# Kernel tuning notes

Hardware: AMD Instinct MI355X
Metric: run time of the kernel (lower is better)

Reference implementation:

```python
import jax, jax.numpy as jnp
import numpy as np

N_USER, N_ITEM = 100000, 50000
E, L = 640000, 200000
F0, F1, F2 = 128, 128, 64


def _mean_agg(x_src, src, dst, n_dst):
    # gather messages from source nodes, mean-aggregate onto destination nodes
    msg = x_src[src]                                            # [E, F]
    s = jax.ops.segment_sum(msg, dst, num_segments=n_dst)       # [n_dst, F]
    cnt = jax.ops.segment_sum(jnp.ones((src.shape[0], 1), x_src.dtype), dst,
                              num_segments=n_dst)               # [n_dst, 1]
    return s / jnp.maximum(cnt, 1.0)


def _sage(x_src, x_dst, src, dst, n_dst, Wl, b, Wr):
    # PyG SAGEConv: lin_l(mean_aggr(x_src)) + lin_r(x_dst)
    agg = _mean_agg(x_src, src, dst, n_dst)
    return agg @ Wl + b + x_dst @ Wr


def setup_inputs() -> dict:
    key = jax.random.key(0)
    ks = jax.random.split(key, 20)
    inp = {}
    inp['x_user'] = jax.random.normal(ks[0], (N_USER, F0), jnp.float32)
    inp['x_item'] = jax.random.normal(ks[1], (N_ITEM, F0), jnp.float32)
    inp['src_u'] = jax.random.randint(ks[2], (E,), 0, N_USER)
    inp['dst_i'] = jax.random.randint(ks[3], (E,), 0, N_ITEM)
    inp['el_src'] = jax.random.randint(ks[4], (L,), 0, N_USER)
    inp['el_dst'] = jax.random.randint(ks[5], (L,), 0, N_ITEM)
    # SAGEConv params per edge type per layer: Wl (neighbor), bias, Wr (root)
    def w(k, fi, fo):
        return jax.random.normal(k, (fi, fo), jnp.float32) * (1.0 / np.sqrt(fi))
    inp['Wl_ui1'] = w(ks[6], F0, F1);  inp['b_ui1'] = jnp.zeros((F1,), jnp.float32)
    inp['Wr_ui1'] = w(ks[7], F0, F1)
    inp['Wl_iu1'] = w(ks[8], F0, F1);  inp['b_iu1'] = jnp.zeros((F1,), jnp.float32)
    inp['Wr_iu1'] = w(ks[9], F0, F1)
    inp['Wl_ui2'] = w(ks[10], F1, F2); inp['b_ui2'] = jnp.zeros((F2,), jnp.float32)
    inp['Wr_ui2'] = w(ks[11], F1, F2)
    inp['Wl_iu2'] = w(ks[12], F1, F2); inp['b_iu2'] = jnp.zeros((F2,), jnp.float32)
    inp['Wr_iu2'] = w(ks[13], F1, F2)
    return inp


def reference(x_user, x_item, src_u, dst_i, el_src, el_dst,
              Wl_ui1, b_ui1, Wr_ui1, Wl_iu1, b_iu1, Wr_iu1,
              Wl_ui2, b_ui2, Wr_ui2, Wl_iu2, b_iu2, Wr_iu2):
    # layer 1 (to_hetero: one SAGEConv per edge type; relu per node type; eval -> no dropout)
    h_i1 = jax.nn.relu(_sage(x_user, x_item, src_u, dst_i, N_ITEM, Wl_ui1, b_ui1, Wr_ui1))
    h_u1 = jax.nn.relu(_sage(x_item, x_user, dst_i, src_u, N_USER, Wl_iu1, b_iu1, Wr_iu1))
    # layer 2
    h_i2 = _sage(h_u1, h_i1, src_u, dst_i, N_ITEM, Wl_ui2, b_ui2, Wr_ui2)
    h_u2 = _sage(h_i1, h_u1, dst_i, src_u, N_USER, Wl_iu2, b_iu2, Wr_iu2)
    # LPsimple_classif: gather endpoints, elementwise product, sum over features
    pred = (h_u2[el_src] * h_i2[el_dst]).sum(axis=-1)           # [L]
    return pred
```

## Files before the change

### kernel.cpp

```cpp
#include <hip/hip_runtime.h>

#define NUSER 100000
#define NITEM 50000
#define NEDGE 640000
#define NLINK 200000
#define GI 49
#define GU 98

typedef unsigned int  uint;
typedef unsigned short ushort_t;
typedef __attribute__((ext_vector_type(8))) short bf16x8;
typedef __attribute__((ext_vector_type(4))) float f32x4;
typedef __attribute__((ext_vector_type(4))) uint  u32x4;

__device__ __forceinline__ ushort_t f2bf(float f) {
    uint u = __float_as_uint(f);
    u += 0x7FFFu + ((u >> 16) & 1u);
    return (ushort_t)(u >> 16);
}
__device__ __forceinline__ float bf2f(ushort_t h) { return __uint_as_float(((uint)h) << 16); }
__device__ __forceinline__ float lo16f(uint u) { return __uint_as_float(u << 16); }
__device__ __forceinline__ float hi16f(uint u) { return __uint_as_float(u & 0xFFFF0000u); }

__global__ __launch_bounds__(256) void countw_kernel(
    const int* __restrict__ src, const int* __restrict__ dst,
    int* __restrict__ cnt_u, int* __restrict__ cnt_i,
    const float* __restrict__ Wl0, const float* __restrict__ Wr0,
    const float* __restrict__ Wl1, const float* __restrict__ Wr1,
    const float* __restrict__ Wl2, const float* __restrict__ Wr2,
    const float* __restrict__ Wl3, const float* __restrict__ Wr3,
    ushort_t* __restrict__ Bh0, ushort_t* __restrict__ Bl0,
    ushort_t* __restrict__ Bh1, ushort_t* __restrict__ Bl1,
    ushort_t* __restrict__ Bh2, ushort_t* __restrict__ Bl2,
    ushort_t* __restrict__ Bh3, ushort_t* __restrict__ Bl3)
{
    if (blockIdx.x < 2500) {
        int e = blockIdx.x * 256 + threadIdx.x;
        if (e >= NEDGE) return;
        atomicAdd(&cnt_u[src[e]], 1);
        atomicAdd(&cnt_i[dst[e]], 1);
        return;
    }
    int b = blockIdx.x - 2500;
    const float *Wl, *Wr; ushort_t *Bh, *Bl; int FO, t;
    if (b < 16)      { Wl = Wl0; Wr = Wr0; Bh = Bh0; Bl = Bl0; FO = 128; t = b * 256 + threadIdx.x; }
    else if (b < 32) { Wl = Wl1; Wr = Wr1; Bh = Bh1; Bl = Bl1; FO = 128; t = (b - 16) * 256 + threadIdx.x; }
    else if (b < 40) { Wl = Wl2; Wr = Wr2; Bh = Bh2; Bl = Bl2; FO = 64;  t = (b - 32) * 256 + threadIdx.x; }
    else             { Wl = Wl3; Wr = Wr3; Bh = Bh3; Bl = Bl3; FO = 64;  t = (b - 40) * 256 + threadIdx.x; }
    int lane = t & 63, ks = (t >> 6) & 3, nt = t >> 8;
    int col = nt * 16 + (lane & 15);
    int k0 = ks * 32 + (lane >> 4) * 8;
    const float* W = (col < FO) ? Wl : Wr;
    int cc = (col < FO) ? col : col - FO;
#pragma unroll
    for (int j = 0; j < 8; ++j) {
        float v = W[(size_t)(k0 + j) * FO + cc];
        ushort_t h = f2bf(v);
        Bh[(size_t)t * 8 + j] = h;
        Bl[(size_t)t * 8 + j] = f2bf(v - bf2f(h));
    }
}

__global__ __launch_bounds__(256) void scan1_kernel(
    const int* __restrict__ cnt_i, const int* __restrict__ cnt_u,
    int* __restrict__ head_i, int* __restrict__ head_u,
    int* __restrict__ bsum_i, int* __restrict__ bsum_u)
{
    __shared__ int sh[256];
    int b = blockIdx.x, t = threadIdx.x;
    const int* cnt; int* head; int* bsum; int n, cb;
    if (b < GI) { cnt = cnt_i; head = head_i; bsum = bsum_i; n = NITEM; cb = b; }
    else        { cnt = cnt_u; head = head_u; bsum = bsum_u; n = NUSER; cb = b - GI; }
    int base = cb * 1024 + t * 4;
    int4 v = {0, 0, 0, 0};
    if (base + 3 < n) v = *(const int4*)(cnt + base);
    else {
        if (base + 0 < n) v.x = cnt[base + 0];
        if (base + 1 < n) v.y = cnt[base + 1];
        if (base + 2 < n) v.z = cnt[base + 2];
    }
    int s = v.x + v.y + v.z + v.w;
    sh[t] = s;
    __syncthreads();
    for (int o = 1; o < 256; o <<= 1) {
        int a = (t >= o) ? sh[t - o] : 0;
        __syncthreads();
        sh[t] += a;
        __syncthreads();
    }
    int excl = sh[t] - s;
    if (t == 255) bsum[cb] = sh[255];
    if (base + 0 < n) head[base + 0] = excl;
    if (base + 1 < n) head[base + 1] = excl + v.x;
    if (base + 2 < n) head[base + 2] = excl + v.x + v.y;
    if (base + 3 < n) head[base + 3] = excl + v.x + v.y + v.z;
}

__global__ __launch_bounds__(256) void scan23_kernel(
    int* __restrict__ head_i, int* __restrict__ head_u,
    const int* __restrict__ bsum_i, const int* __restrict__ bsum_u)
{
    __shared__ int sh[256];
    int b = blockIdx.x, t = threadIdx.x;
    int* head; const int* bsum; int n, cb;
    if (b < GI) { head = head_i; bsum = bsum_i; n = NITEM; cb = b; }
    else        { head = head_u; bsum = bsum_u; n = NUSER; cb = b - GI; }
    sh[t] = (t < cb) ? bsum[t] : 0;
    __syncthreads();
    for (int o = 128; o >= 1; o >>= 1) {
        if (t < o) sh[t] += sh[t + o];
        __syncthreads();
    }
    int add = sh[0];
    int base = cb * 1024 + t * 4;
#pragma unroll
    for (int k = 0; k < 4; ++k)
        if (base + k < n) head[base + k] += add;
}

#define FCHUNK 2048
#define FNCH   313
#define NBG1   4688
__global__ __launch_bounds__(256) void gemmfill_kernel(
    const float* __restrict__ xu, const float* __restrict__ xi,
    const ushort_t* __restrict__ Bh0, const ushort_t* __restrict__ Bl0,
    const ushort_t* __restrict__ Bh1, const ushort_t* __restrict__ Bl1,
    ushort_t* __restrict__ y0, ushort_t* __restrict__ z0,
    ushort_t* __restrict__ y1, ushort_t* __restrict__ z1,
    const int* __restrict__ src, const int* __restrict__ dst,
    int* __restrict__ head_i, int* __restrict__ head_u,
    int* __restrict__ nbr_i, int* __restrict__ nbr_u)
{
    if (blockIdx.x >= NBG1) {
        int b = blockIdx.x - NBG1;
        int pass = b / (2 * FNCH);
        int rem  = b % (2 * FNCH);
        int dir  = rem / FNCH;
        int base = (rem % FNCH) * FCHUNK;
        int e_end = min(base + FCHUNK, NEDGE);
        if (dir == 0) {
            int lo = pass * (NITEM / 8), hi = lo + NITEM / 8;
            for (int e = base + threadIdx.x; e < e_end; e += 256) {
                int d = dst[e];
                if (d >= lo && d < hi) nbr_i[atomicAdd(&head_i[d], 1)] = src[e];
            }
        } else {
            int lo = pass * (NUSER / 8), hi = lo + NUSER / 8;
            for (int e = base + threadIdx.x; e < e_end; e += 256) {
                int s = src[e];
                if (s >= lo && s < hi) nbr_u[atomicAdd(&head_u[s], 1)] = dst[e];
            }
        }
        return;
    }

    __shared__ u32x4 ashH[32][16];
    __shared__ u32x4 ashL[32][16];
    const int tid = threadIdx.x;
    const float* A; const ushort_t *Bh, *Bl; ushort_t *ymsg, *zout; int n, row0;
    if ((int)blockIdx.x < 3125) { A = xu; Bh = Bh0; Bl = Bl0; ymsg = y0; zout = z0; n = NUSER; row0 = blockIdx.x * 32; }
    else { A = xi; Bh = Bh1; Bl = Bl1; ymsg = y1; zout = z1; n = NITEM; row0 = (blockIdx.x - 3125) * 32; }

#pragma unroll
    for (int i = 0; i < 2; ++i) {
        int idx = i * 256 + tid;
        int row = idx >> 4, ch = idx & 15;
        int grow = row0 + row;
        f32x4 f0 = {0.f, 0.f, 0.f, 0.f}, f1 = {0.f, 0.f, 0.f, 0.f};
        if (grow < n) {
            const f32x4* p = (const f32x4*)(A + (size_t)grow * 128 + ch * 8);
            f0 = p[0]; f1 = p[1];
        }
        float e[8];
#pragma unroll
        for (int j = 0; j < 4; ++j) { e[j] = f0[j]; e[4 + j] = f1[j]; }
        uint hv[4], lv[4];
#pragma unroll
        for (int j = 0; j < 4; ++j) {
            ushort_t h0 = f2bf(e[2 * j]), h1 = f2bf(e[2 * j + 1]);
            hv[j] = (uint)h0 | ((uint)h1 << 16);
            ushort_t l0 = f2bf(e[2 * j] - bf2f(h0)), l1 = f2bf(e[2 * j + 1] - bf2f(h1));
            lv[j] = (uint)l0 | ((uint)l1 << 16);
        }
        int sc = ch ^ (row & 7);
        u32x4 hq = {hv[0], hv[1], hv[2], hv[3]};
        u32x4 lq = {lv[0], lv[1], lv[2], lv[3]};
        ashH[row][sc] = hq;
        ashL[row][sc] = lq;
    }
    __syncthreads();

    const int lane = tid & 63, wv = tid >> 6;
    const int lr = lane & 15, lg = lane >> 4;
    const int colbase = wv * 64;
    f32x4 acc[2][4];
#pragma unroll
    for (int rt = 0; rt < 2; ++rt)
#pragma unroll
        for (int ct = 0; ct < 4; ++ct) { f32x4 zz = {0.f, 0.f, 0.f, 0.f}; acc[rt][ct] = zz; }

#pragma unroll
    for (int ks = 0; ks < 4; ++ks) {
        bf16x8 ah[2], al[2];
#pragma unroll
        for (int rt = 0; rt < 2; ++rt) {
            int row = rt * 16 + lr;
            int pos = (ks * 4 + lg) ^ (row & 7);
            ah[rt] = __builtin_bit_cast(bf16x8, ashH[row][pos]);
            al[rt] = __builtin_bit_cast(bf16x8, ashL[row][pos]);
        }
#pragma unroll
        for (int ct = 0; ct < 4; ++ct) {
            int nt = (colbase >> 4) + ct;
            size_t off = ((size_t)(nt * 4 + ks) * 64 + lane) * 8;
            bf16x8 bh = __builtin_bit_cast(bf16x8, *(const u32x4*)(Bh + off));
            bf16x8 bl = __builtin_bit_cast(bf16x8, *(const u32x4*)(Bl + off));
#pragma unroll
            for (int rt = 0; rt < 2; ++rt) {
                acc[rt][ct] = __builtin_amdgcn_mfma_f32_16x16x32_bf16(ah[rt], bh, acc[rt][ct], 0, 0, 0);
                acc[rt][ct] = __builtin_amdgcn_mfma_f32_16x16x32_bf16(ah[rt], bl, acc[rt][ct], 0, 0, 0);
                acc[rt][ct] = __builtin_amdgcn_mfma_f32_16x16x32_bf16(al[rt], bh, acc[rt][ct], 0, 0, 0);
            }
        }
    }

#pragma unroll
    for (int rt = 0; rt < 2; ++rt)
#pragma unroll
        for (int ct = 0; ct < 4; ++ct) {
            int col = colbase + ct * 16 + lr;
            bool ism = col < 128;
            ushort_t* dstp = ism ? ymsg : zout;
            int cc = ism ? col : col - 128;
#pragma unroll
            for (int r = 0; r < 4; ++r) {
                int row = row0 + rt * 16 + lg * 4 + r;
                if (row < n) dstp[(size_t)row * 128 + cc] = f2bf(acc[rt][ct][r]);
            }
        }
}

__global__ __launch_bounds__(256) void gemm2_kernel(
    const ushort_t* __restrict__ A0, const ushort_t* __restrict__ A1,
    const ushort_t* __restrict__ Bh0, const ushort_t* __restrict__ Bl0,
    const ushort_t* __restrict__ Bh1, const ushort_t* __restrict__ Bl1,
    ushort_t* __restrict__ y0, ushort_t* __restrict__ z0,
    ushort_t* __restrict__ y1, ushort_t* __restrict__ z1,
    int n0, int n1, int nb0)
{
    __shared__ u32x4 ashH[32][16];
    const int tid = threadIdx.x;
    const ushort_t* A; const ushort_t *Bh, *Bl; ushort_t *ymsg, *zout; int n, row0;
    if ((int)blockIdx.x < nb0) { A = A0; Bh = Bh0; Bl = Bl0; ymsg = y0; zout = z0; n = n0; row0 = blockIdx.x * 32; }
    else { A = A1; Bh = Bh1; Bl = Bl1; ymsg = y1; zout = z1; n = n1; row0 = (blockIdx.x - nb0) * 32; }

#pragma unroll
    for (int i = 0; i < 2; ++i) {
        int idx = i * 256 + tid;
        int row = idx >> 4, ch = idx & 15;
        int grow = row0 + row;
        u32x4 q = {0u, 0u, 0u, 0u};
        if (grow < n) q = *(const u32x4*)(A + (size_t)grow * 128 + ch * 8);
        ashH[row][ch ^ (row & 7)] = q;
    }
    __syncthreads();

    const int lane = tid & 63, wv = tid >> 6;
    const int lr = lane & 15, lg = lane >> 4;
    const int colbase = wv * 32;
    f32x4 acc[2][2];
#pragma unroll
    for (int rt = 0; rt < 2; ++rt)
#pragma unroll
        for (int ct = 0; ct < 2; ++ct) { f32x4 zz = {0.f, 0.f, 0.f, 0.f}; acc[rt][ct] = zz; }

#pragma unroll
    for (int ks = 0; ks < 4; ++ks) {
        bf16x8 ah[2];
#pragma unroll
        for (int rt = 0; rt < 2; ++rt) {
            int row = rt * 16 + lr;
            int pos = (ks * 4 + lg) ^ (row & 7);
            ah[rt] = __builtin_bit_cast(bf16x8, ashH[row][pos]);
        }
#pragma unroll
        for (int ct = 0; ct < 2; ++ct) {
            int nt = (colbase >> 4) + ct;
            size_t off = ((size_t)(nt * 4 + ks) * 64 + lane) * 8;
            bf16x8 bh = __builtin_bit_cast(bf16x8, *(const u32x4*)(Bh + off));
            bf16x8 bl = __builtin_bit_cast(bf16x8, *(const u32x4*)(Bl + off));
#pragma unroll
            for (int rt = 0; rt < 2; ++rt) {
                acc[rt][ct] = __builtin_amdgcn_mfma_f32_16x16x32_bf16(ah[rt], bh, acc[rt][ct], 0, 0, 0);
                acc[rt][ct] = __builtin_amdgcn_mfma_f32_16x16x32_bf16(ah[rt], bl, acc[rt][ct], 0, 0, 0);
            }
        }
    }

#pragma unroll
    for (int rt = 0; rt < 2; ++rt)
#pragma unroll
        for (int ct = 0; ct < 2; ++ct) {
            int col = colbase + ct * 16 + lr;
            bool ism = col < 64;
            ushort_t* dstp = ism ? ymsg : zout;
            int cc = ism ? col : col - 64;
#pragma unroll
            for (int r = 0; r < 4; ++r) {
                int row = row0 + rt * 16 + lg * 4 + r;
                if (row < n) dstp[(size_t)row * 64 + cc] = f2bf(acc[rt][ct][r]);
            }
        }
}

__global__ __launch_bounds__(256) void gather1_kernel(
    const ushort_t* __restrict__ ymsg_u, const ushort_t* __restrict__ ymsg_i,
    const int* __restrict__ nbr_i, const int* __restrict__ head_i, const int* __restrict__ cnt_i,
    const int* __restrict__ nbr_u, const int* __restrict__ head_u, const int* __restrict__ cnt_u,
    const ushort_t* __restrict__ z_i, const ushort_t* __restrict__ z_u,
    const float* __restrict__ b_ui, const float* __restrict__ b_iu,
    ushort_t* __restrict__ h1_i, ushort_t* __restrict__ h1_u)
{
    int w = (blockIdx.x << 2) + (threadIdx.x >> 6);
    const ushort_t *ym, *z; const int *nbr, *head, *cnt; const float* bias;
    ushort_t* hout; int node;
    if (w < NITEM) { ym = ymsg_u; nbr = nbr_i; head = head_i; cnt = cnt_i; z = z_i; bias = b_ui; hout = h1_i; node = w; }
    else if (w < NITEM + NUSER) { ym = ymsg_i; nbr = nbr_u; head = head_u; cnt = cnt_u; z = z_u; bias = b_iu; hout = h1_u; node = w - NITEM; }
    else return;
    int lane = threadIdx.x & 63;
    int c = cnt[node], end = head[node];
    int j = end - c;
    const uint* Y = (const uint*)ym;
    float ax = 0.f, ay = 0.f;
    for (; j + 7 < end; j += 8) {
        uint u0 = Y[(size_t)nbr[j + 0] * 64 + lane];
        uint u1 = Y[(size_t)nbr[j + 1] * 64 + lane];
        uint u2 = Y[(size_t)nbr[j + 2] * 64 + lane];
        uint u3 = Y[(size_t)nbr[j + 3] * 64 + lane];
        uint u4 = Y[(size_t)nbr[j + 4] * 64 + lane];
        uint u5 = Y[(size_t)nbr[j + 5] * 64 + lane];
        uint u6 = Y[(size_t)nbr[j + 6] * 64 + lane];
        uint u7 = Y[(size_t)nbr[j + 7] * 64 + lane];
        ax += lo16f(u0) + lo16f(u1) + lo16f(u2) + lo16f(u3)
            + lo16f(u4) + lo16f(u5) + lo16f(u6) + lo16f(u7);
        ay += hi16f(u0) + hi16f(u1) + hi16f(u2) + hi16f(u3)
            + hi16f(u4) + hi16f(u5) + hi16f(u6) + hi16f(u7);
    }
    for (; j + 1 < end; j += 2) {
        uint u0 = Y[(size_t)nbr[j + 0] * 64 + lane];
        uint u1 = Y[(size_t)nbr[j + 1] * 64 + lane];
        ax += lo16f(u0) + lo16f(u1);
        ay += hi16f(u0) + hi16f(u1);
    }
    if (j < end) {
        uint u0 = Y[(size_t)nbr[j] * 64 + lane];
        ax += lo16f(u0); ay += hi16f(u0);
    }
    float m = 1.f / fmaxf((float)c, 1.f);
    uint zu = ((const uint*)z)[(size_t)node * 64 + lane];
    float vx = fmaxf(ax * m + lo16f(zu) + bias[lane * 2], 0.f);
    float vy = fmaxf(ay * m + hi16f(zu) + bias[lane * 2 + 1], 0.f);
    ((uint*)hout)[(size_t)node * 64 + lane] = (uint)f2bf(vx) | ((uint)f2bf(vy) << 16);
}

__global__ __launch_bounds__(256) void gather2_kernel(
    const ushort_t* __restrict__ ymsg_u, const ushort_t* __restrict__ ymsg_i,
    const int* __restrict__ nbr_i, const int* __restrict__ head_i, const int* __restrict__ cnt_i,
    const int* __restrict__ nbr_u, const int* __restrict__ head_u, const int* __restrict__ cnt_u,
    const ushort_t* __restrict__ z_i, const ushort_t* __restrict__ z_u,
    const float* __restrict__ b_ui, const float* __restrict__ b_iu,
    ushort_t* __restrict__ h2_i, ushort_t* __restrict__ h2_u)
{
    int w = (blockIdx.x << 2) + (threadIdx.x >> 6);
    const ushort_t *ym, *z; const int *nbr, *head, *cnt; const float* bias;
    ushort_t* hout; int node;
    if (w < NITEM) { ym = ymsg_u; nbr = nbr_i; head = head_i; cnt = cnt_i; z = z_i; bias = b_ui; hout = h2_i; node = w; }
    else if (w < NITEM + NUSER) { ym = ymsg_i; nbr = nbr_u; head = head_u; cnt = cnt_u; z = z_u; bias = b_iu; hout = h2_u; node = w - NITEM; }
    else return;
    int lane = threadIdx.x & 63;
    int c = cnt[node], end = head[node];
    int j = end - c;
    float a = 0.f;
    for (; j + 7 < end; j += 8) {
        a += bf2f(ym[(size_t)nbr[j + 0] * 64 + lane]) + bf2f(ym[(size_t)nbr[j + 1] * 64 + lane])
           + bf2f(ym[(size_t)nbr[j + 2] * 64 + lane]) + bf2f(ym[(size_t)nbr[j + 3] * 64 + lane])
           + bf2f(ym[(size_t)nbr[j + 4] * 64 + lane]) + bf2f(ym[(size_t)nbr[j + 5] * 64 + lane])
           + bf2f(ym[(size_t)nbr[j + 6] * 64 + lane]) + bf2f(ym[(size_t)nbr[j + 7] * 64 + lane]);
    }
    for (; j + 1 < end; j += 2)
        a += bf2f(ym[(size_t)nbr[j] * 64 + lane]) + bf2f(ym[(size_t)nbr[j + 1] * 64 + lane]);
    if (j < end) a += bf2f(ym[(size_t)nbr[j] * 64 + lane]);
    float m = 1.f / fmaxf((float)c, 1.f);
    float v = a * m + bf2f(z[(size_t)node * 64 + lane]) + bias[lane];
    hout[(size_t)node * 64 + lane] = f2bf(v);
}

__global__ __launch_bounds__(256) void predict_kernel(
    const int* __restrict__ el_src, const int* __restrict__ el_dst,
    const ushort_t* __restrict__ hu, const ushort_t* __restrict__ hi,
    float* __restrict__ out)
{
    int l = (blockIdx.x << 2) + (threadIdx.x >> 6);
    if (l >= NLINK) return;
    int lane = threadIdx.x & 63;
    int u = el_src[l];
    int it = el_dst[l];
    float v = bf2f(hu[(size_t)u * 64 + lane]) * bf2f(hi[(size_t)it * 64 + lane]);
#pragma unroll
    for (int o = 32; o >= 1; o >>= 1) v += __shfl_down(v, o, 64);
    if (lane == 0) out[l] = v;
}

extern "C" void kernel_launch(void* const* d_in, const int* in_sizes, int n_in,
                              void* d_out, int out_size, void* d_ws, size_t ws_size,
                              hipStream_t stream) {
    const float* x_user = (const float*)d_in[0];
    const float* x_item = (const float*)d_in[1];
    const int*   src_u  = (const int*)d_in[2];
    const int*   dst_i  = (const int*)d_in[3];
    const int*   el_src = (const int*)d_in[4];
    const int*   el_dst = (const int*)d_in[5];
    const float* Wl_ui1 = (const float*)d_in[6];
    const float* b_ui1  = (const float*)d_in[7];
    const float* Wr_ui1 = (const float*)d_in[8];
    const float* Wl_iu1 = (const float*)d_in[9];
    const float* b_iu1  = (const float*)d_in[10];
    const float* Wr_iu1 = (const float*)d_in[11];
    const float* Wl_ui2 = (const float*)d_in[12];
    const float* b_ui2  = (const float*)d_in[13];
    const float* Wr_ui2 = (const float*)d_in[14];
    const float* Wl_iu2 = (const float*)d_in[15];
    const float* b_iu2  = (const float*)d_in[16];
    const float* Wr_iu2 = (const float*)d_in[17];
    float* out = (float*)d_out;

    int* iw     = (int*)d_ws;
    int* cnt_i  = iw;
    int* cnt_u  = iw + 50000;
    int* bsum_i = iw + 150000;
    int* bsum_u = iw + 150064;
    int* head_i = iw + 150192;
    int* head_u = iw + 200192;
    int* nbr_i  = iw + 300192;
    int* nbr_u  = iw + 940192;
    char* W8 = (char*)d_ws;
    size_t off = 6320768;
    ushort_t* Bh1u = (ushort_t*)(W8 + off); off += 65536;
    ushort_t* Bl1u = (ushort_t*)(W8 + off); off += 65536;
    ushort_t* Bh1i = (ushort_t*)(W8 + off); off += 65536;
    ushort_t* Bl1i = (ushort_t*)(W8 + off); off += 65536;
    ushort_t* Bh2u = (ushort_t*)(W8 + off); off += 32768;
    ushort_t* Bl2u = (ushort_t*)(W8 + off); off += 32768;
    ushort_t* Bh2i = (ushort_t*)(W8 + off); off += 32768;
    ushort_t* Bl2i = (ushort_t*)(W8 + off); off += 32768;
    ushort_t* h1_u = (ushort_t*)(W8 + off); off += (size_t)NUSER * 128 * 2;
    ushort_t* h1_i = (ushort_t*)(W8 + off); off += (size_t)NITEM * 128 * 2;
    size_t YB = off;
    ushort_t* ymsg_u = (ushort_t*)(W8 + YB);
    ushort_t* ymsg_i = (ushort_t*)(W8 + YB + 25600000);
    ushort_t* z_u    = (ushort_t*)(W8 + YB + 38400000);
    ushort_t* z_i    = (ushort_t*)(W8 + YB + 64000000);
    ushort_t* ymsg2_u = (ushort_t*)(W8 + YB);
    ushort_t* ymsg2_i = (ushort_t*)(W8 + YB + 12800000);
    ushort_t* z2_u    = (ushort_t*)(W8 + YB + 19200000);
    ushort_t* z2_i    = (ushort_t*)(W8 + YB + 32000000);
    ushort_t* h2_u    = (ushort_t*)(W8 + YB + 38400000);
    ushort_t* h2_i    = (ushort_t*)(W8 + YB + 51200000);

    hipMemsetAsync(d_ws, 0, 150000 * sizeof(int), stream);

    countw_kernel<<<2548, 256, 0, stream>>>(
        src_u, dst_i, cnt_u, cnt_i,
        Wl_ui1, Wr_iu1, Wl_iu1, Wr_ui1, Wl_ui2, Wr_iu2, Wl_iu2, Wr_ui2,
        Bh1u, Bl1u, Bh1i, Bl1i, Bh2u, Bl2u, Bh2i, Bl2i);

    scan1_kernel<<<GI + GU, 256, 0, stream>>>(cnt_i, cnt_u, head_i, head_u, bsum_i, bsum_u);
    scan23_kernel<<<GI + GU, 256, 0, stream>>>(head_i, head_u, bsum_i, bsum_u);

    gemmfill_kernel<<<NBG1 + 8 * 2 * FNCH, 256, 0, stream>>>(
        x_user, x_item, Bh1u, Bl1u, Bh1i, Bl1i,
        ymsg_u, z_u, ymsg_i, z_i,
        src_u, dst_i, head_i, head_u, nbr_i, nbr_u);

    gather1_kernel<<<(NITEM + NUSER) / 4, 256, 0, stream>>>(
        ymsg_u, ymsg_i, nbr_i, head_i, cnt_i, nbr_u, head_u, cnt_u,
        z_i, z_u, b_ui1, b_iu1, h1_i, h1_u);

    gemm2_kernel<<<3125 + 1563, 256, 0, stream>>>(
        h1_u, h1_i, Bh2u, Bl2u, Bh2i, Bl2i,
        ymsg2_u, z2_u, ymsg2_i, z2_i, NUSER, NITEM, 3125);
    gather2_kernel<<<(NITEM + NUSER) / 4, 256, 0, stream>>>(
        ymsg2_u, ymsg2_i, nbr_i, head_i, cnt_i, nbr_u, head_u, cnt_u,
        z2_i, z2_u, b_ui2, b_iu2, h2_i, h2_u);

    predict_kernel<<<NLINK / 4, 256, 0, stream>>>(el_src, el_dst, h2_u, h2_i, out);
}
```

Before: 353.5 us.

## Make GEMM blocks persistent over 128 rows with register-resident weights and prefetch

Both GEMM kernels now use 512-thread blocks, each looping over four 32-row sub-tiles (128 rows total). The split-bf16 weight fragments are loaded into registers once per block instead of being reloaded per 32-row tile, and the next sub-tile's activations are prefetched while the current one runs through MFMA. The edge-fill path uses larger chunks and 512-thread strides to match. Weight fragments held in registers raise VGPR pressure, which may lower occupancy, and the grid shrinks to about 1173 GEMM blocks.

```diff
diff --git a/kernel.cpp b/kernel.cpp
--- a/kernel.cpp
+++ b/kernel.cpp
@@ -6,6 +6,11 @@
 #define NLINK 200000
 #define GI 49
 #define GU 98
+#define NBU1 782
+#define NBI1 391
+#define NBG1 (NBU1 + NBI1)
+#define FCHUNK 4096
+#define FNCH 157
 
 typedef unsigned int  uint;
 typedef unsigned short ushort_t;
@@ -118,10 +123,127 @@
         if (base + k < n) head[base + k] += add;
 }
 
-#define FCHUNK 2048
-#define FNCH   313
-#define NBG1   4688
-__global__ __launch_bounds__(256) void gemmfill_kernel(
+template <int NO, bool ASPLIT>
+__device__ __forceinline__ void gemm_body(
+    const void* __restrict__ A_,
+    const ushort_t* __restrict__ Bh, const ushort_t* __restrict__ Bl,
+    ushort_t* __restrict__ ymsg, ushort_t* __restrict__ zout,
+    int n, int row0, u32x4 (*ashH)[16], u32x4 (*ashL)[16])
+{
+    constexpr int CT = NO / 128;
+    constexpr int FO = NO / 2;
+    const int tid = threadIdx.x;
+    const int lane = tid & 63, wv = tid >> 6;
+    const int lr = lane & 15, lg = lane >> 4;
+    const int row = tid >> 4, ch = tid & 15;
+
+    bf16x8 bfh[4][CT], bfl[4][CT];
+#pragma unroll
+    for (int ks = 0; ks < 4; ++ks)
+#pragma unroll
+        for (int ct = 0; ct < CT; ++ct) {
+            size_t boff = ((size_t)((wv * CT + ct) * 4 + ks) * 64 + lane) * 8;
+            bfh[ks][ct] = __builtin_bit_cast(bf16x8, *(const u32x4*)(Bh + boff));
+            bfl[ks][ct] = __builtin_bit_cast(bf16x8, *(const u32x4*)(Bl + boff));
+        }
+
+    f32x4 c0 = {0.f, 0.f, 0.f, 0.f}, c1 = {0.f, 0.f, 0.f, 0.f};
+    u32x4 cq = {0u, 0u, 0u, 0u};
+    {
+        int grow = row0 + row;
+        if (grow < n) {
+            if (ASPLIT) {
+                const f32x4* p = (const f32x4*)((const float*)A_ + (size_t)grow * 128 + ch * 8);
+                c0 = p[0]; c1 = p[1];
+            } else {
+                cq = *(const u32x4*)((const ushort_t*)A_ + (size_t)grow * 128 + ch * 8);
+            }
+        }
+    }
+
+#pragma unroll
+    for (int st = 0; st < 4; ++st) {
+        int sc = ch ^ (row & 7);
+        if (ASPLIT) {
+            float e[8];
+#pragma unroll
+            for (int j = 0; j < 4; ++j) { e[j] = c0[j]; e[4 + j] = c1[j]; }
+            uint hv[4], lv[4];
+#pragma unroll
+            for (int j = 0; j < 4; ++j) {
+                ushort_t h0 = f2bf(e[2 * j]), h1 = f2bf(e[2 * j + 1]);
+                hv[j] = (uint)h0 | ((uint)h1 << 16);
+                ushort_t l0 = f2bf(e[2 * j] - bf2f(h0)), l1 = f2bf(e[2 * j + 1] - bf2f(h1));
+                lv[j] = (uint)l0 | ((uint)l1 << 16);
+            }
+            u32x4 hq = {hv[0], hv[1], hv[2], hv[3]};
+            u32x4 lq = {lv[0], lv[1], lv[2], lv[3]};
+            ashH[row][sc] = hq;
+            ashL[row][sc] = lq;
+        } else {
+            ashH[row][sc] = cq;
+        }
+        __syncthreads();
+
+        if (st < 3) {
+            c0 = f32x4{0.f, 0.f, 0.f, 0.f}; c1 = f32x4{0.f, 0.f, 0.f, 0.f};
+            cq = u32x4{0u, 0u, 0u, 0u};
+            int grow = row0 + (st + 1) * 32 + row;
+            if (grow < n) {
+                if (ASPLIT) {
+                    const f32x4* p = (const f32x4*)((const float*)A_ + (size_t)grow * 128 + ch * 8);
+                    c0 = p[0]; c1 = p[1];
+                } else {
+                    cq = *(const u32x4*)((const ushort_t*)A_ + (size_t)grow * 128 + ch * 8);
+                }
+            }
+        }
+
+        f32x4 acc[2][CT];
+#pragma unroll
+        for (int rt = 0; rt < 2; ++rt)
+#pragma unroll
+            for (int ct = 0; ct < CT; ++ct) { f32x4 zz = {0.f, 0.f, 0.f, 0.f}; acc[rt][ct] = zz; }
+#pragma unroll
+        for (int ks = 0; ks < 4; ++ks) {
+            bf16x8 ah[2], al[2];
+#pragma unroll
+            for (int rt = 0; rt < 2; ++rt) {
+                int arow = rt * 16 + lr;
+                int pos = (ks * 4 + lg) ^ (arow & 7);
+                ah[rt] = __builtin_bit_cast(bf16x8, ashH[arow][pos]);
+                if (ASPLIT) al[rt] = __builtin_bit_cast(bf16x8, ashL[arow][pos]);
+            }
+#pragma unroll
+            for (int ct = 0; ct < CT; ++ct)
+#pragma unroll
+                for (int rt = 0; rt < 2; ++rt) {
+                    acc[rt][ct] = __builtin_amdgcn_mfma_f32_16x16x32_bf16(ah[rt], bfh[ks][ct], acc[rt][ct], 0, 0, 0);
+                    acc[rt][ct] = __builtin_amdgcn_mfma_f32_16x16x32_bf16(ah[rt], bfl[ks][ct], acc[rt][ct], 0, 0, 0);
+                    if (ASPLIT)
+                        acc[rt][ct] = __builtin_amdgcn_mfma_f32_16x16x32_bf16(al[rt], bfh[ks][ct], acc[rt][ct], 0, 0, 0);
+                }
+        }
+
+#pragma unroll
+        for (int rt = 0; rt < 2; ++rt)
+#pragma unroll
+            for (int ct = 0; ct < CT; ++ct) {
+                int col = wv * (NO / 8) + ct * 16 + lr;
+                bool ism = col < FO;
+                ushort_t* dstp = ism ? ymsg : zout;
+                int cc = ism ? col : col - FO;
+#pragma unroll
+                for (int r = 0; r < 4; ++r) {
+                    int orow = row0 + st * 32 + rt * 16 + lg * 4 + r;
+                    if (orow < n) dstp[(size_t)orow * FO + cc] = f2bf(acc[rt][ct][r]);
+                }
+            }
+        __syncthreads();
+    }
+}
+
+__global__ __launch_bounds__(512) void gemmfill_kernel(
     const float* __restrict__ xu, const float* __restrict__ xi,
     const ushort_t* __restrict__ Bh0, const ushort_t* __restrict__ Bl0,
     const ushort_t* __restrict__ Bh1, const ushort_t* __restrict__ Bl1,
@@ -140,177 +262,39 @@
         int e_end = min(base + FCHUNK, NEDGE);
         if (dir == 0) {
             int lo = pass * (NITEM / 8), hi = lo + NITEM / 8;
-            for (int e = base + threadIdx.x; e < e_end; e += 256) {
+            for (int e = base + threadIdx.x; e < e_end; e += 512) {
                 int d = dst[e];
                 if (d >= lo && d < hi) nbr_i[atomicAdd(&head_i[d], 1)] = src[e];
             }
         } else {
             int lo = pass * (NUSER / 8), hi = lo + NUSER / 8;
-            for (int e = base + threadIdx.x; e < e_end; e += 256) {
+            for (int e = base + threadIdx.x; e < e_end; e += 512) {
                 int s = src[e];
                 if (s >= lo && s < hi) nbr_u[atomicAdd(&head_u[s], 1)] = dst[e];
             }
         }
         return;
     }
-
     __shared__ u32x4 ashH[32][16];
     __shared__ u32x4 ashL[32][16];
-    const int tid = threadIdx.x;
-    const float* A; const ushort_t *Bh, *Bl; ushort_t *ymsg, *zout; int n, row0;
-    if ((int)blockIdx.x < 3125) { A = xu; Bh = Bh0; Bl = Bl0; ymsg = y0; zout = z0; n = NUSER; row0 = blockIdx.x * 32; }
-    else { A = xi; Bh = Bh1; Bl = Bl1; ymsg = y1; zout = z1; n = NITEM; row0 = (blockIdx.x - 3125) * 32; }
-
-#pragma unroll
-    for (int i = 0; i < 2; ++i) {
-        int idx = i * 256 + tid;
-        int row = idx >> 4, ch = idx & 15;
-        int grow = row0 + row;
-        f32x4 f0 = {0.f, 0.f, 0.f, 0.f}, f1 = {0.f, 0.f, 0.f, 0.f};
-        if (grow < n) {
-            const f32x4* p = (const f32x4*)(A + (size_t)grow * 128 + ch * 8);
-            f0 = p[0]; f1 = p[1];
-        }
-        float e[8];
-#pragma unroll
-        for (int j = 0; j < 4; ++j) { e[j] = f0[j]; e[4 + j] = f1[j]; }
-        uint hv[4], lv[4];
-#pragma unroll
-        for (int j = 0; j < 4; ++j) {
-            ushort_t h0 = f2bf(e[2 * j]), h1 = f2bf(e[2 * j + 1]);
-            hv[j] = (uint)h0 | ((uint)h1 << 16);
-            ushort_t l0 = f2bf(e[2 * j] - bf2f(h0)), l1 = f2bf(e[2 * j + 1] - bf2f(h1));
-            lv[j] = (uint)l0 | ((uint)l1 << 16);
-        }
-        int sc = ch ^ (row & 7);
-        u32x4 hq = {hv[0], hv[1], hv[2], hv[3]};
-        u32x4 lq = {lv[0], lv[1], lv[2], lv[3]};
-        ashH[row][sc] = hq;
-        ashL[row][sc] = lq;
-    }
-    __syncthreads();
-
-    const int lane = tid & 63, wv = tid >> 6;
-    const int lr = lane & 15, lg = lane >> 4;
-    const int colbase = wv * 64;
-    f32x4 acc[2][4];
-#pragma unroll
-    for (int rt = 0; rt < 2; ++rt)
-#pragma unroll
-        for (int ct = 0; ct < 4; ++ct) { f32x4 zz = {0.f, 0.f, 0.f, 0.f}; acc[rt][ct] = zz; }
-
-#pragma unroll
-    for (int ks = 0; ks < 4; ++ks) {
-        bf16x8 ah[2], al[2];
-#pragma unroll
-        for (int rt = 0; rt < 2; ++rt) {
-            int row = rt * 16 + lr;
-            int pos = (ks * 4 + lg) ^ (row & 7);
-            ah[rt] = __builtin_bit_cast(bf16x8, ashH[row][pos]);
-            al[rt] = __builtin_bit_cast(bf16x8, ashL[row][pos]);
-        }
-#pragma unroll
-        for (int ct = 0; ct < 4; ++ct) {
-            int nt = (colbase >> 4) + ct;
-            size_t off = ((size_t)(nt * 4 + ks) * 64 + lane) * 8;
-            bf16x8 bh = __builtin_bit_cast(bf16x8, *(const u32x4*)(Bh + off));
-            bf16x8 bl = __builtin_bit_cast(bf16x8, *(const u32x4*)(Bl + off));
-#pragma unroll
-            for (int rt = 0; rt < 2; ++rt) {
-                acc[rt][ct] = __builtin_amdgcn_mfma_f32_16x16x32_bf16(ah[rt], bh, acc[rt][ct], 0, 0, 0);
-                acc[rt][ct] = __builtin_amdgcn_mfma_f32_16x16x32_bf16(ah[rt], bl, acc[rt][ct], 0, 0, 0);
-                acc[rt][ct] = __builtin_amdgcn_mfma_f32_16x16x32_bf16(al[rt], bh, acc[rt][ct], 0, 0, 0);
-            }
-        }
-    }
-
-#pragma unroll
-    for (int rt = 0; rt < 2; ++rt)
-#pragma unroll
-        for (int ct = 0; ct < 4; ++ct) {
-            int col = colbase + ct * 16 + lr;
-            bool ism = col < 128;
-            ushort_t* dstp = ism ? ymsg : zout;
-            int cc = ism ? col : col - 128;
-#pragma unroll
-            for (int r = 0; r < 4; ++r) {
-                int row = row0 + rt * 16 + lg * 4 + r;
-                if (row < n) dstp[(size_t)row * 128 + cc] = f2bf(acc[rt][ct][r]);
-            }
-        }
-}
-
-__global__ __launch_bounds__(256) void gemm2_kernel(
+    if ((int)blockIdx.x < NBU1)
+        gemm_body<256, true>(xu, Bh0, Bl0, y0, z0, NUSER, blockIdx.x * 128, ashH, ashL);
+    else
+        gemm_body<256, true>(xi, Bh1, Bl1, y1, z1, NITEM, (blockIdx.x - NBU1) * 128, ashH, ashL);
+}
+
+__global__ __launch_bounds__(512) void gemm2_kernel(
     const ushort_t* __restrict__ A0, const ushort_t* __restrict__ A1,
     const ushort_t* __restrict__ Bh0, const ushort_t* __restrict__ Bl0,
     const ushort_t* __restrict__ Bh1, const ushort_t* __restrict__ Bl1,
     ushort_t* __restrict__ y0, ushort_t* __restrict__ z0,
-    ushort_t* __restrict__ y1, ushort_t* __restrict__ z1,
-    int n0, int n1, int nb0)
+    ushort_t* __restrict__ y1, ushort_t* __restrict__ z1)
 {
     __shared__ u32x4 ashH[32][16];
-    const int tid = threadIdx.x;
-    const ushort_t* A; const ushort_t *Bh, *Bl; ushort_t *ymsg, *zout; int n, row0;
-    if ((int)blockIdx.x < nb0) { A = A0; Bh = Bh0; Bl = Bl0; ymsg = y0; zout = z0; n = n0; row0 = blockIdx.x * 32; }
-    else { A = A1; Bh = Bh1; Bl = Bl1; ymsg = y1; zout = z1; n = n1; row0 = (blockIdx.x - nb0) * 32; }
-
-#pragma unroll
-    for (int i = 0; i < 2; ++i) {
-        int idx = i * 256 + tid;
-        int row = idx >> 4, ch = idx & 15;
-        int grow = row0 + row;
-        u32x4 q = {0u, 0u, 0u, 0u};
-        if (grow < n) q = *(const u32x4*)(A + (size_t)grow * 128 + ch * 8);
-        ashH[row][ch ^ (row & 7)] = q;
-    }
-    __syncthreads();
-
-    const int lane = tid & 63, wv = tid >> 6;
-    const int lr = lane & 15, lg = lane >> 4;
-    const int colbase = wv * 32;
-    f32x4 acc[2][2];
-#pragma unroll
-    for (int rt = 0; rt < 2; ++rt)
-#pragma unroll
-        for (int ct = 0; ct < 2; ++ct) { f32x4 zz = {0.f, 0.f, 0.f, 0.f}; acc[rt][ct] = zz; }
-
-#pragma unroll
-    for (int ks = 0; ks < 4; ++ks) {
-        bf16x8 ah[2];
-#pragma unroll
-        for (int rt = 0; rt < 2; ++rt) {
-            int row = rt * 16 + lr;
-            int pos = (ks * 4 + lg) ^ (row & 7);
-            ah[rt] = __builtin_bit_cast(bf16x8, ashH[row][pos]);
-        }
-#pragma unroll
-        for (int ct = 0; ct < 2; ++ct) {
-            int nt = (colbase >> 4) + ct;
-            size_t off = ((size_t)(nt * 4 + ks) * 64 + lane) * 8;
-            bf16x8 bh = __builtin_bit_cast(bf16x8, *(const u32x4*)(Bh + off));
-            bf16x8 bl = __builtin_bit_cast(bf16x8, *(const u32x4*)(Bl + off));
-#pragma unroll
-            for (int rt = 0; rt < 2; ++rt) {
-                acc[rt][ct] = __builtin_amdgcn_mfma_f32_16x16x32_bf16(ah[rt], bh, acc[rt][ct], 0, 0, 0);
-                acc[rt][ct] = __builtin_amdgcn_mfma_f32_16x16x32_bf16(ah[rt], bl, acc[rt][ct], 0, 0, 0);
-            }
-        }
-    }
-
-#pragma unroll
-    for (int rt = 0; rt < 2; ++rt)
-#pragma unroll
-        for (int ct = 0; ct < 2; ++ct) {
-            int col = colbase + ct * 16 + lr;
-            bool ism = col < 64;
-            ushort_t* dstp = ism ? ymsg : zout;
-            int cc = ism ? col : col - 64;
-#pragma unroll
-            for (int r = 0; r < 4; ++r) {
-                int row = row0 + rt * 16 + lg * 4 + r;
-                if (row < n) dstp[(size_t)row * 64 + cc] = f2bf(acc[rt][ct][r]);
-            }
-        }
+    if ((int)blockIdx.x < NBU1)
+        gemm_body<128, false>(A0, Bh0, Bl0, y0, z0, NUSER, blockIdx.x * 128, ashH, ashH);
+    else
+        gemm_body<128, false>(A1, Bh1, Bl1, y1, z1, NITEM, (blockIdx.x - NBU1) * 128, ashH, ashH);
 }
 
 __global__ __launch_bounds__(256) void gather1_kernel(
@@ -477,7 +461,7 @@
     scan1_kernel<<<GI + GU, 256, 0, stream>>>(cnt_i, cnt_u, head_i, head_u, bsum_i, bsum_u);
     scan23_kernel<<<GI + GU, 256, 0, stream>>>(head_i, head_u, bsum_i, bsum_u);
 
-    gemmfill_kernel<<<NBG1 + 8 * 2 * FNCH, 256, 0, stream>>>(
+    gemmfill_kernel<<<NBG1 + 8 * 2 * FNCH, 512, 0, stream>>>(
         x_user, x_item, Bh1u, Bl1u, Bh1i, Bl1i,
         ymsg_u, z_u, ymsg_i, z_i,
         src_u, dst_i, head_i, head_u, nbr_i, nbr_u);
@@ -486,9 +470,9 @@
         ymsg_u, ymsg_i, nbr_i, head_i, cnt_i, nbr_u, head_u, cnt_u,
         z_i, z_u, b_ui1, b_iu1, h1_i, h1_u);
 
-    gemm2_kernel<<<3125 + 1563, 256, 0, stream>>>(
+    gemm2_kernel<<<NBG1, 512, 0, stream>>>(
         h1_u, h1_i, Bh2u, Bl2u, Bh2i, Bl2i,
-        ymsg2_u, z2_u, ymsg2_i, z2_i, NUSER, NITEM, 3125);
+        ymsg2_u, z2_u, ymsg2_i, z2_i);
     gather2_kernel<<<(NITEM + NUSER) / 4, 256, 0, stream>>>(
         ymsg2_u, ymsg2_i, nbr_i, head_i, cnt_i, nbr_u, head_u, cnt_u,
         z2_i, z2_u, b_ui2, b_iu2, h2_i, h2_u);
```

New measurement: 363.6 us. 1.03x slower.
